# Kernel tuning notes

Hardware: AMD Instinct MI355X
Metric: run time of the kernel (lower is better)

## Reference

```python
import jax, jax.numpy as jnp
import numpy as np

# ---- config constants (from ResidualNetConfig) ----
BOUND_LO = jnp.array([-5.0, -5.0, -5.0], dtype=jnp.float32)
BOUND_DIS = jnp.array([10.0, 10.0, 10.0], dtype=jnp.float32)
N_MIN = 200                 # int(ceil(max extent)/resolution) = 10/0.05
PER_LEVEL_SCALE = 2.0
NUM_LEVELS = 4
LOG2_T = 19
T = 1 << LOG2_T
OUTPUT_SDF_SCALE = 0.1
LEAKY_SLOPE = 0.01

# Instant-NGP spatial hash primes (first coord uses 1)
PRIMES = (np.uint32(1), np.uint32(2654435761), np.uint32(805459861))
# 8 corner offsets of the unit cube, [8, 3]
CORNERS = jnp.array([[(c >> d) & 1 for d in range(3)] for c in range(8)], dtype=jnp.uint32)


def hash_grid_encode(xyz01, tables):
    """xyz01: [N,3] in [0,1]; tables: [L,T,F] -> [N, L*F] trilinear hashed features."""
    feats = []
    for l in range(NUM_LEVELS):
        res = jnp.float32(N_MIN * (PER_LEVEL_SCALE ** l))
        pos = xyz01 * res                       # [N,3]
        pfloor = jnp.floor(pos)
        frac = pos - pfloor                     # [N,3]
        base = pfloor.astype(jnp.uint32)        # [N,3]
        corner = base[:, None, :] + CORNERS[None, :, :]   # [N,8,3]
        h = (corner[..., 0] * PRIMES[0]) ^ (corner[..., 1] * PRIMES[1]) ^ (corner[..., 2] * PRIMES[2])
        idx = (h & jnp.uint32(T - 1)).astype(jnp.int32)   # [N,8]
        f = tables[l][idx]                      # [N,8,F] irregular gather
        # trilinear weights: prod over dims of frac (corner=1) or 1-frac (corner=0)
        w = jnp.prod(jnp.where(CORNERS[None].astype(bool), frac[:, None, :], 1.0 - frac[:, None, :]), axis=-1)  # [N,8]
        feats.append(jnp.sum(f * w[..., None], axis=1))   # [N,F]
    return jnp.concatenate(feats, axis=-1)      # [N, L*F]


def leaky_relu(x):
    return jnp.where(x >= 0, x, LEAKY_SLOPE * x)


def setup_inputs() -> dict:
    key = jax.random.key(0)
    k1, k2, k3, k4, k5 = jax.random.split(key, 5)
    N = 2_000_000
    xyz = jax.random.uniform(k1, (N, 3), dtype=jnp.float32) * BOUND_DIS + BOUND_LO
    tables = jax.random.normal(k2, (NUM_LEVELS, T, 2), dtype=jnp.float32) * 1e-2
    W_in = jax.random.normal(k3, (8, 64), dtype=jnp.float32) / np.sqrt(8.0)
    W_h = jax.random.normal(k4, (64, 64), dtype=jnp.float32) / np.sqrt(64.0)
    W_out = jax.random.normal(k5, (64, 1), dtype=jnp.float32) / np.sqrt(64.0)
    return {"xyz": xyz, "tables": tables, "W_in": W_in, "W_h": W_h, "W_out": W_out}


def reference(xyz, tables, W_in, W_h, W_out):
    # scale_with_bound: map xyz into [0,1]^3
    xyz01 = (xyz - BOUND_LO) / BOUND_DIS
    enc = hash_grid_encode(xyz01, tables)        # [N, 8]
    h = leaky_relu(enc @ W_in)                   # hidden layer 1
    h = leaky_relu(h @ W_h)                      # hidden layer 2
    sdf = (h @ W_out).reshape(-1) * OUTPUT_SDF_SCALE
    return sdf
```

## Files before the change

### kernel.cpp

```cpp
#include <hip/hip_runtime.h>
#include <hip/hip_fp16.h>

static constexpr unsigned TSIZE = 1u << 19;
static constexpr unsigned TMASK = TSIZE - 1u;

typedef _Float16 f16;
typedef f16   f16x8 __attribute__((ext_vector_type(8)));
typedef float f32x4 __attribute__((ext_vector_type(4)));

union H2U { __half2 h; unsigned u; };

__global__ __launch_bounds__(256)
void cvt_tables(const float4* __restrict__ in, __half2* __restrict__ out, int n4)
{
    int i = blockIdx.x * 256 + threadIdx.x;
    if (i < n4) {
        float4 v = in[i];
        out[2 * i]     = __floats2half2_rn(v.x, v.y);
        out[2 * i + 1] = __floats2half2_rn(v.z, v.w);
    }
}

struct HashIssue {
    uint2    pv[4];
    unsigned uodd[4];
    unsigned flags;
    float    frx, fry, frz;
};

__device__ __forceinline__ HashIssue hash_issue(float px, float py, float pz, int l,
                                                const __half2* __restrict__ tab)
{
    HashIssue r;
    const float res = 200.0f * (float)(1 << l);
    const float fx = px * res, fy = py * res, fz = pz * res;
    const float flx = floorf(fx), fly = floorf(fy), flz = floorf(fz);
    r.frx = fx - flx; r.fry = fy - fly; r.frz = fz - flz;
    const unsigned bx = (unsigned)flx, by = (unsigned)fly, bz = (unsigned)flz;
    const unsigned hy0 = by * 2654435761u, hy1 = (by + 1u) * 2654435761u;
    const unsigned hz0 = bz * 805459861u,  hz1 = (bz + 1u) * 805459861u;
    const unsigned syz[4] = { hy0 ^ hz0, hy1 ^ hz0, hy0 ^ hz1, hy1 ^ hz1 };
    const uint2* __restrict__ tabp = (const uint2*)tab;

    unsigned flags = (bx & 1u) << 4;
    #pragma unroll
    for (int p = 0; p < 4; ++p) {
        const unsigned i0 = (bx ^ syz[p]) & TMASK;
        r.pv[p] = tabp[i0 >> 1];
        flags |= (i0 & 1u) << p;
        r.uodd[p] = 0u;
    }
    if (bx & 1u) {
        #pragma unroll
        for (int p = 0; p < 4; ++p) {
            const unsigned i1 = ((bx + 1u) ^ syz[p]) & TMASK;
            H2U t; t.h = tab[i1];
            r.uodd[p] = t.u;
        }
    }
    r.flags = flags;
    return r;
}

__device__ __forceinline__ void hash_blend(const HashIssue& r, float& e0, float& e1)
{
    const float wx0 = 1.0f - r.frx, wx1 = r.frx;
    const float wyv[2] = {1.0f - r.fry, r.fry};
    const float wzv[2] = {1.0f - r.frz, r.frz};
    const bool bxodd = (r.flags >> 4) & 1u;
    e0 = 0.0f; e1 = 0.0f;
    #pragma unroll
    for (int p = 0; p < 4; ++p) {
        const bool sw = (r.flags >> p) & 1u;
        unsigned a = sw ? r.pv[p].y : r.pv[p].x;
        unsigned b = sw ? r.pv[p].x : r.pv[p].y;
        b = bxodd ? r.uodd[p] : b;
        H2U ua, ub; ua.u = a; ub.u = b;
        const float2 f0 = __half22float2(ua.h);
        const float2 f1 = __half22float2(ub.h);
        const float wyz = wyv[p & 1] * wzv[(p >> 1) & 1];
        e0 = fmaf(fmaf(f1.x, wx1, f0.x * wx0), wyz, e0);
        e1 = fmaf(fmaf(f1.y, wx1, f0.y * wx0), wyz, e1);
    }
}

__device__ __forceinline__ void stage_xyz(const float* __restrict__ xyz, int bbase, int N,
                                          float* sxyz, float& px, float& py, float& pz)
{
    const int g3 = bbase * 3;
    #pragma unroll
    for (int t = 0; t < 3; ++t) {
        int sidx = (int)threadIdx.x + t * 256;
        int g = g3 + sidx;
        sxyz[sidx] = (g < 3 * N) ? __builtin_nontemporal_load(&xyz[g]) : 0.0f;
    }
    __syncthreads();
    px = (sxyz[threadIdx.x * 3 + 0] + 5.0f) * 0.1f;
    py = (sxyz[threadIdx.x * 3 + 1] + 5.0f) * 0.1f;
    pz = (sxyz[threadIdx.x * 3 + 2] + 5.0f) * 0.1f;
}

__global__ __launch_bounds__(256, 4)
void encode01(const float* __restrict__ xyz, const __half2* __restrict__ tab16,
              unsigned long long* __restrict__ enc01, int N)
{
    __shared__ float sxyz[768];
    const int bbase = blockIdx.x * 256;
    const int i = bbase + (int)threadIdx.x;
    float px, py, pz;
    stage_xyz(xyz, bbase, N, sxyz, px, py, pz);

    HashIssue h0 = hash_issue(px, py, pz, 0, tab16);
    HashIssue h1 = hash_issue(px, py, pz, 1, tab16 + TSIZE);

    float e0, e1, e2, e3;
    hash_blend(h0, e0, e1);
    hash_blend(h1, e2, e3);

    H2U a, b;
    a.h = __floats2half2_rn(e0, e1);
    b.h = __floats2half2_rn(e2, e3);
    if (i < N) {
        unsigned long long v = (unsigned long long)a.u
                             | ((unsigned long long)b.u << 32);
        __builtin_nontemporal_store(v, &enc01[i]);
    }
}

static constexpr int H1_STRIDE = 72;

__global__ __launch_bounds__(256, 4)
void mlp23_mfma(const float* __restrict__ xyz, const __half2* __restrict__ tab16,
                const unsigned long long* __restrict__ enc01,
                const float* __restrict__ Win, const float* __restrict__ Wh,
                const float* __restrict__ Wout, float* __restrict__ out, int N)
{
    __shared__ float sxyz[768];
    __shared__ f16 h1s[256 * H1_STRIDE];

    const int bbase = blockIdx.x * 256;
    const int i = bbase + (int)threadIdx.x;
    float px, py, pz;
    stage_xyz(xyz, bbase, N, sxyz, px, py, pz);

    const unsigned long long v01 = __builtin_nontemporal_load(&enc01[i < N ? i : 0]);
    HashIssue h2 = hash_issue(px, py, pz, 2, tab16 + 2 * TSIZE);
    HashIssue h3 = hash_issue(px, py, pz, 3, tab16 + 3 * TSIZE);

    float enc[8];
    {
        H2U a, b; a.u = (unsigned)v01; b.u = (unsigned)(v01 >> 32);
        float2 f01 = __half22float2(a.h);
        float2 f23 = __half22float2(b.h);
        enc[0] = f01.x; enc[1] = f01.y; enc[2] = f23.x; enc[3] = f23.y;
    }
    hash_blend(h2, enc[4], enc[5]);
    hash_blend(h3, enc[6], enc[7]);

    float h1[64];
    #pragma unroll
    for (int j = 0; j < 64; ++j) h1[j] = 0.0f;
    #pragma unroll
    for (int k = 0; k < 8; ++k) {
        const float e = enc[k];
        #pragma unroll
        for (int j = 0; j < 64; ++j)
            h1[j] = fmaf(e, Win[k * 64 + j], h1[j]);
    }
    {
        f16* row = &h1s[(int)threadIdx.x * H1_STRIDE];
        #pragma unroll
        for (int jj = 0; jj < 8; ++jj) {
            f16x8 v;
            #pragma unroll
            for (int e = 0; e < 8; ++e) {
                float a = h1[jj * 8 + e];
                a = (a >= 0.0f) ? a : 0.01f * a;
                v[e] = (f16)a;
            }
            *(f16x8*)(row + jj * 8) = v;
        }
    }
    __syncthreads();

    const int wave = (int)threadIdx.x >> 6;
    const int lane = (int)threadIdx.x & 63;
    const int c = lane & 15;
    const int q = lane >> 4;
    const f16* wbase = &h1s[wave * 64 * H1_STRIDE];

    f16x8 bfrag[2][4];
    #pragma unroll
    for (int kt = 0; kt < 2; ++kt)
        #pragma unroll
        for (int nt = 0; nt < 4; ++nt)
            #pragma unroll
            for (int j = 0; j < 8; ++j)
                bfrag[kt][nt][j] = (f16)Wh[(kt * 32 + q * 8 + j) * 64 + nt * 16 + c];

    f32x4 Ct[4][4];
    #pragma unroll
    for (int mt = 0; mt < 4; ++mt)
        #pragma unroll
        for (int nt = 0; nt < 4; ++nt)
            Ct[mt][nt] = (f32x4){0.f, 0.f, 0.f, 0.f};

    #pragma unroll
    for (int mt = 0; mt < 4; ++mt) {
        #pragma unroll
        for (int kt = 0; kt < 2; ++kt) {
            const f16x8 a = *(const f16x8*)&wbase[(mt * 16 + c) * H1_STRIDE + kt * 32 + q * 8];
            #pragma unroll
            for (int nt = 0; nt < 4; ++nt)
                Ct[mt][nt] = __builtin_amdgcn_mfma_f32_16x16x32_f16(a, bfrag[kt][nt], Ct[mt][nt], 0, 0, 0);
        }
    }

    float acc3[4][4];
    #pragma unroll
    for (int mt = 0; mt < 4; ++mt)
        #pragma unroll
        for (int r = 0; r < 4; ++r) acc3[mt][r] = 0.0f;

    #pragma unroll
    for (int nt = 0; nt < 4; ++nt) {
        const float wo = Wout[nt * 16 + c];
        #pragma unroll
        for (int mt = 0; mt < 4; ++mt)
            #pragma unroll
            for (int r = 0; r < 4; ++r) {
                float v = Ct[mt][nt][r];
                v = (v >= 0.0f) ? v : 0.01f * v;
                acc3[mt][r] = fmaf(v, wo, acc3[mt][r]);
            }
    }
    #pragma unroll
    for (int mask = 1; mask <= 8; mask <<= 1)
        #pragma unroll
        for (int mt = 0; mt < 4; ++mt)
            #pragma unroll
            for (int r = 0; r < 4; ++r)
                acc3[mt][r] += __shfl_xor(acc3[mt][r], mask, 64);

    if (c == 0) {
        #pragma unroll
        for (int mt = 0; mt < 4; ++mt)
            #pragma unroll
            for (int r = 0; r < 4; ++r) {
                int p = bbase + wave * 64 + mt * 16 + q * 4 + r;
                if (p < N) out[p] = acc3[mt][r] * 0.1f;
            }
    }
}

__global__ __launch_bounds__(256, 2)
void resnet_mono(const float* __restrict__ xyz, const float* __restrict__ tables,
                 const float* __restrict__ Win, const float* __restrict__ Wh,
                 const float* __restrict__ Wout, float* __restrict__ out, int N)
{
    __shared__ float sxyz[768];
    const int bbase = blockIdx.x * 256;
    const int i = bbase + (int)threadIdx.x;
    float px, py, pz;
    stage_xyz(xyz, bbase, N, sxyz, px, py, pz);

    float enc[8];
    #pragma unroll
    for (int l = 0; l < 4; ++l) {
        const float res = 200.0f * (float)(1 << l);
        const float fx = px * res, fy = py * res, fz = pz * res;
        const float flx = floorf(fx), fly = floorf(fy), flz = floorf(fz);
        const float frx = fx - flx, fry = fy - fly, frz = fz - flz;
        const unsigned bx = (unsigned)flx, by = (unsigned)fly, bz = (unsigned)flz;
        const unsigned hy0 = by * 2654435761u, hy1 = (by + 1u) * 2654435761u;
        const unsigned hz0 = bz * 805459861u,  hz1 = (bz + 1u) * 805459861u;
        const float wx[2] = {1.0f - frx, frx};
        const float wy[2] = {1.0f - fry, fry};
        const float wz[2] = {1.0f - frz, frz};
        const float2* tab = (const float2*)tables + (size_t)l * TSIZE;
        float e0 = 0.0f, e1 = 0.0f;
        #pragma unroll
        for (int cc = 0; cc < 8; ++cc) {
            unsigned h = (bx + (unsigned)(cc & 1))
                       ^ ((cc & 2) ? hy1 : hy0)
                       ^ ((cc & 4) ? hz1 : hz0);
            float2 f = tab[h & TMASK];
            float w = wx[cc & 1] * wy[(cc >> 1) & 1] * wz[(cc >> 2) & 1];
            e0 = fmaf(f.x, w, e0);
            e1 = fmaf(f.y, w, e1);
        }
        enc[2 * l] = e0; enc[2 * l + 1] = e1;
    }

    float h1[64];
    #pragma unroll
    for (int j = 0; j < 64; ++j) h1[j] = 0.0f;
    #pragma unroll
    for (int k = 0; k < 8; ++k) {
        const float e = enc[k];
        #pragma unroll
        for (int j = 0; j < 64; ++j)
            h1[j] = fmaf(e, Win[k * 64 + j], h1[j]);
    }
    #pragma unroll
    for (int j = 0; j < 64; ++j)
        h1[j] = (h1[j] >= 0.0f) ? h1[j] : 0.01f * h1[j];

    float sdf = 0.0f;
    #pragma unroll
    for (int j0 = 0; j0 < 64; j0 += 16) {
        float acc[16];
        #pragma unroll
        for (int jj = 0; jj < 16; ++jj) acc[jj] = 0.0f;
        #pragma unroll
        for (int k = 0; k < 64; ++k) {
            const float hk = h1[k];
            #pragma unroll
            for (int jj = 0; jj < 16; ++jj)
                acc[jj] = fmaf(hk, Wh[k * 64 + j0 + jj], acc[jj]);
        }
        #pragma unroll
        for (int jj = 0; jj < 16; ++jj) {
            float a = acc[jj];
            a = (a >= 0.0f) ? a : 0.01f * a;
            sdf = fmaf(a, Wout[j0 + jj], sdf);
        }
    }
    if (i < N) out[i] = sdf * 0.1f;
}

extern "C" void kernel_launch(void* const* d_in, const int* in_sizes, int n_in,
                              void* d_out, int out_size, void* d_ws, size_t ws_size,
                              hipStream_t stream) {
    const float* xyz    = (const float*)d_in[0];
    const float* tables = (const float*)d_in[1];
    const float* Win    = (const float*)d_in[2];
    const float* Wh     = (const float*)d_in[3];
    const float* Wout   = (const float*)d_in[4];
    float* out = (float*)d_out;

    const int N = in_sizes[0] / 3;
    const int blocks = (N + 255) / 256;

    const int tab_floats = in_sizes[1];
    const size_t tab16_bytes = (size_t)tab_floats * 2;
    const size_t enc01_bytes = (size_t)N * 8;

    if (ws_size >= tab16_bytes + enc01_bytes) {
        __half2* tab16 = (__half2*)d_ws;
        unsigned long long* enc01 = (unsigned long long*)((char*)d_ws + tab16_bytes);
        int n4 = tab_floats / 4;
        hipLaunchKernelGGL(cvt_tables, dim3((n4 + 255) / 256), dim3(256), 0, stream,
                           (const float4*)tables, tab16, n4);
        hipLaunchKernelGGL(encode01, dim3(blocks), dim3(256), 0, stream,
                           xyz, tab16, enc01, N);
        hipLaunchKernelGGL(mlp23_mfma, dim3(blocks), dim3(256), 0, stream,
                           xyz, tab16, enc01, Win, Wh, Wout, out, N);
    } else {
        hipLaunchKernelGGL(resnet_mono, dim3(blocks), dim3(256), 0, stream,
                           xyz, tables, Win, Wh, Wout, out, N);
    }
}
```

Measured before the change: 328.7 us.

## Fuse encode and MLP kernels, pipeline hash levels, swizzle LDS layout

Merges the two-kernel split (levels 0-1 encode written to a workspace buffer, then levels 2-3 plus MLP) into one fused kernel that computes all four hash levels in software-pipelined pairs. This removes the intermediate enc01 write and read and one kernel launch. The padded LDS stride of 72 is replaced with an XOR-swizzled 64-wide layout to avoid bank conflicts. xyz is now loaded directly per thread instead of being staged through shared memory. The cost is more gather latency concentrated in one kernel, which may weaken latency hiding compared with the split design.

```diff
diff --git a/kernel.cpp b/kernel.cpp
--- a/kernel.cpp
+++ b/kernel.cpp
@@ -84,78 +84,30 @@
     }
 }
 
-__device__ __forceinline__ void stage_xyz(const float* __restrict__ xyz, int bbase, int N,
-                                          float* sxyz, float& px, float& py, float& pz)
-{
-    const int g3 = bbase * 3;
-    #pragma unroll
-    for (int t = 0; t < 3; ++t) {
-        int sidx = (int)threadIdx.x + t * 256;
-        int g = g3 + sidx;
-        sxyz[sidx] = (g < 3 * N) ? __builtin_nontemporal_load(&xyz[g]) : 0.0f;
-    }
-    __syncthreads();
-    px = (sxyz[threadIdx.x * 3 + 0] + 5.0f) * 0.1f;
-    py = (sxyz[threadIdx.x * 3 + 1] + 5.0f) * 0.1f;
-    pz = (sxyz[threadIdx.x * 3 + 2] + 5.0f) * 0.1f;
-}
-
 __global__ __launch_bounds__(256, 4)
-void encode01(const float* __restrict__ xyz, const __half2* __restrict__ tab16,
-              unsigned long long* __restrict__ enc01, int N)
-{
-    __shared__ float sxyz[768];
+void resnet_fused(const float* __restrict__ xyz, const __half2* __restrict__ tab16,
+                  const float* __restrict__ Win, const float* __restrict__ Wh,
+                  const float* __restrict__ Wout, float* __restrict__ out, int N)
+{
+    __shared__ f16 h1s[256 * 64];
+
     const int bbase = blockIdx.x * 256;
     const int i = bbase + (int)threadIdx.x;
-    float px, py, pz;
-    stage_xyz(xyz, bbase, N, sxyz, px, py, pz);
-
-    HashIssue h0 = hash_issue(px, py, pz, 0, tab16);
-    HashIssue h1 = hash_issue(px, py, pz, 1, tab16 + TSIZE);
-
-    float e0, e1, e2, e3;
-    hash_blend(h0, e0, e1);
-    hash_blend(h1, e2, e3);
-
-    H2U a, b;
-    a.h = __floats2half2_rn(e0, e1);
-    b.h = __floats2half2_rn(e2, e3);
-    if (i < N) {
-        unsigned long long v = (unsigned long long)a.u
-                             | ((unsigned long long)b.u << 32);
-        __builtin_nontemporal_store(v, &enc01[i]);
-    }
-}
-
-static constexpr int H1_STRIDE = 72;
-
-__global__ __launch_bounds__(256, 4)
-void mlp23_mfma(const float* __restrict__ xyz, const __half2* __restrict__ tab16,
-                const unsigned long long* __restrict__ enc01,
-                const float* __restrict__ Win, const float* __restrict__ Wh,
-                const float* __restrict__ Wout, float* __restrict__ out, int N)
-{
-    __shared__ float sxyz[768];
-    __shared__ f16 h1s[256 * H1_STRIDE];
-
-    const int bbase = blockIdx.x * 256;
-    const int i = bbase + (int)threadIdx.x;
-    float px, py, pz;
-    stage_xyz(xyz, bbase, N, sxyz, px, py, pz);
-
-    const unsigned long long v01 = __builtin_nontemporal_load(&enc01[i < N ? i : 0]);
-    HashIssue h2 = hash_issue(px, py, pz, 2, tab16 + 2 * TSIZE);
-    HashIssue h3 = hash_issue(px, py, pz, 3, tab16 + 3 * TSIZE);
+    const int ci = (i < N) ? i : (N - 1);
+
+    const float px = (__builtin_nontemporal_load(&xyz[ci * 3 + 0]) + 5.0f) * 0.1f;
+    const float py = (__builtin_nontemporal_load(&xyz[ci * 3 + 1]) + 5.0f) * 0.1f;
+    const float pz = (__builtin_nontemporal_load(&xyz[ci * 3 + 2]) + 5.0f) * 0.1f;
 
     float enc[8];
-    {
-        H2U a, b; a.u = (unsigned)v01; b.u = (unsigned)(v01 >> 32);
-        float2 f01 = __half22float2(a.h);
-        float2 f23 = __half22float2(b.h);
-        enc[0] = f01.x; enc[1] = f01.y; enc[2] = f23.x; enc[3] = f23.y;
-    }
-    hash_blend(h2, enc[4], enc[5]);
-    hash_blend(h3, enc[6], enc[7]);
+    HashIssue ha = hash_issue(px, py, pz, 0, tab16);
+    HashIssue hb = hash_issue(px, py, pz, 1, tab16 + TSIZE);
+    hash_blend(ha, enc[0], enc[1]);
+    ha = hash_issue(px, py, pz, 2, tab16 + 2 * TSIZE);
+    hash_blend(hb, enc[2], enc[3]);
+    hb = hash_issue(px, py, pz, 3, tab16 + 3 * TSIZE);
+    hash_blend(ha, enc[4], enc[5]);
+    hash_blend(hb, enc[6], enc[7]);
 
     float h1[64];
     #pragma unroll
@@ -168,7 +120,8 @@
             h1[j] = fmaf(e, Win[k * 64 + j], h1[j]);
     }
     {
-        f16* row = &h1s[(int)threadIdx.x * H1_STRIDE];
+        char* base = (char*)h1s;
+        const int row = (int)threadIdx.x;
         #pragma unroll
         for (int jj = 0; jj < 8; ++jj) {
             f16x8 v;
@@ -178,7 +131,8 @@
                 a = (a >= 0.0f) ? a : 0.01f * a;
                 v[e] = (f16)a;
             }
-            *(f16x8*)(row + jj * 8) = v;
+            const int byteoff = (row * 128 + jj * 16) ^ ((row & 7) << 4);
+            *(f16x8*)(base + byteoff) = v;
         }
     }
     __syncthreads();
@@ -187,7 +141,6 @@
     const int lane = (int)threadIdx.x & 63;
     const int c = lane & 15;
     const int q = lane >> 4;
-    const f16* wbase = &h1s[wave * 64 * H1_STRIDE];
 
     f16x8 bfrag[2][4];
     #pragma unroll
@@ -205,11 +158,14 @@
         for (int nt = 0; nt < 4; ++nt)
             Ct[mt][nt] = (f32x4){0.f, 0.f, 0.f, 0.f};
 
+    const char* base = (const char*)h1s;
     #pragma unroll
     for (int mt = 0; mt < 4; ++mt) {
         #pragma unroll
         for (int kt = 0; kt < 2; ++kt) {
-            const f16x8 a = *(const f16x8*)&wbase[(mt * 16 + c) * H1_STRIDE + kt * 32 + q * 8];
+            const int row = wave * 64 + mt * 16 + c;
+            const int byteoff = (row * 128 + kt * 64 + q * 16) ^ ((row & 7) << 4);
+            const f16x8 a = *(const f16x8*)(base + byteoff);
             #pragma unroll
             for (int nt = 0; nt < 4; ++nt)
                 Ct[mt][nt] = __builtin_amdgcn_mfma_f32_16x16x32_f16(a, bfrag[kt][nt], Ct[mt][nt], 0, 0, 0);
@@ -258,11 +214,12 @@
                  const float* __restrict__ Win, const float* __restrict__ Wh,
                  const float* __restrict__ Wout, float* __restrict__ out, int N)
 {
-    __shared__ float sxyz[768];
     const int bbase = blockIdx.x * 256;
     const int i = bbase + (int)threadIdx.x;
-    float px, py, pz;
-    stage_xyz(xyz, bbase, N, sxyz, px, py, pz);
+    const int ci = (i < N) ? i : (N - 1);
+    const float px = (xyz[ci * 3 + 0] + 5.0f) * 0.1f;
+    const float py = (xyz[ci * 3 + 1] + 5.0f) * 0.1f;
+    const float pz = (xyz[ci * 3 + 2] + 5.0f) * 0.1f;
 
     float enc[8];
     #pragma unroll
@@ -344,18 +301,14 @@
 
     const int tab_floats = in_sizes[1];
     const size_t tab16_bytes = (size_t)tab_floats * 2;
-    const size_t enc01_bytes = (size_t)N * 8;
-
-    if (ws_size >= tab16_bytes + enc01_bytes) {
+
+    if (ws_size >= tab16_bytes) {
         __half2* tab16 = (__half2*)d_ws;
-        unsigned long long* enc01 = (unsigned long long*)((char*)d_ws + tab16_bytes);
         int n4 = tab_floats / 4;
         hipLaunchKernelGGL(cvt_tables, dim3((n4 + 255) / 256), dim3(256), 0, stream,
                            (const float4*)tables, tab16, n4);
-        hipLaunchKernelGGL(encode01, dim3(blocks), dim3(256), 0, stream,
-                           xyz, tab16, enc01, N);
-        hipLaunchKernelGGL(mlp23_mfma, dim3(blocks), dim3(256), 0, stream,
-                           xyz, tab16, enc01, Win, Wh, Wout, out, N);
+        hipLaunchKernelGGL(resnet_fused, dim3(blocks), dim3(256), 0, stream,
+                           xyz, tab16, Win, Wh, Wout, out, N);
     } else {
         hipLaunchKernelGGL(resnet_mono, dim3(blocks), dim3(256), 0, stream,
                            xyz, tables, Win, Wh, Wout, out, N);
```

New measurement: 390.2 us. +18.7%, slower.
